# Optimization experiments

Measured on AMD Instinct MI355X. Metric: run time of the kernel, lower is better.

The kernel has to match this reference:

```python
import jax, jax.numpy as jnp
import numpy as np

N, T, D, H = 32, 1024, 1152, 16
DH = D // H            # 72
MLP = int(D * 4.0)     # 4608
EPS = 1e-6


def setup_inputs() -> dict:
    key = jax.random.key(0)
    ks = jax.random.split(key, 14)
    s = 0.02
    return {
        "x": jax.random.normal(ks[0], (N, T, D), jnp.float32),
        "c": jax.random.normal(ks[1], (N, D), jnp.float32),
        "qkv_w": jax.random.normal(ks[2], (D, 3 * D), jnp.float32) * s,
        "qkv_b": jax.random.normal(ks[3], (3 * D,), jnp.float32) * s,
        "proj_w": jax.random.normal(ks[4], (D, D), jnp.float32) * s,
        "proj_b": jax.random.normal(ks[5], (D,), jnp.float32) * s,
        "fc1_w": jax.random.normal(ks[6], (D, MLP), jnp.float32) * s,
        "fc1_b": jax.random.normal(ks[7], (MLP,), jnp.float32) * s,
        "fc2_w": jax.random.normal(ks[8], (MLP, D), jnp.float32) * s,
        "fc2_b": jax.random.normal(ks[9], (D,), jnp.float32) * s,
        "ada_w": jax.random.normal(ks[10], (D, 6 * D), jnp.float32) * s,
        "ada_b": jax.random.normal(ks[11], (6 * D,), jnp.float32) * s,
    }


def _layernorm(x):
    m = jnp.mean(x, axis=-1, keepdims=True)
    v = jnp.var(x, axis=-1, keepdims=True)
    return (x - m) * jax.lax.rsqrt(v + EPS)


def _modulate(x, shift, scale):
    # shift, scale: (N, D) broadcast over T
    return x * (1.0 + scale[:, None, :]) + shift[:, None, :]


def _attention(x, qkv_w, qkv_b, proj_w, proj_b):
    n, t, d = x.shape
    scale = DH ** (-0.5)
    qkv = x @ qkv_w + qkv_b                       # (N,T,3D)
    qkv = qkv.reshape(n, t, 3, H, DH)
    q, k, v = qkv[:, :, 0], qkv[:, :, 1], qkv[:, :, 2]  # each (N,T,H,DH)
    # Faithful to source: matmul over the LAST two dims -> per-token
    # head-vs-head attention of shape (N,T,H,H), softmax over heads.
    attn = jnp.einsum("nthd,ntkd->nthk", q * scale, k)
    attn = jax.nn.softmax(attn, axis=-1)
    out = jnp.einsum("nthk,ntkd->nthd", attn, v)  # (N,T,H,DH)
    out = out.transpose(0, 2, 1, 3).reshape(n, t, d)  # faithful scramble
    return out @ proj_w + proj_b


def _mlp(x, fc1_w, fc1_b, fc2_w, fc2_b):
    h = jax.nn.gelu(x @ fc1_w + fc1_b, approximate=False)  # exact GELU (torch default)
    return h @ fc2_w + fc2_b


def reference(x, c, qkv_w, qkv_b, proj_w, proj_b, fc1_w, fc1_b, fc2_w, fc2_b,
              ada_w, ada_b):
    ada = jax.nn.silu(c) @ ada_w + ada_b          # (N, 6D)
    (shift_msa, scale_msa, gate_msa,
     shift_mlp, scale_mlp, gate_mlp) = jnp.split(ada, 6, axis=1)
    x = x + gate_msa[:, None, :] * _attention(
        _modulate(_layernorm(x), shift_msa, scale_msa),
        qkv_w, qkv_b, proj_w, proj_b)
    x = x + gate_mlp[:, None, :] * _mlp(
        _modulate(_layernorm(x), shift_mlp, scale_mlp),
        fc1_w, fc1_b, fc2_w, fc2_b)
    return x
```

## Files before the change

kernel.cpp:

```cpp
#include <hip/hip_runtime.h>

#define DEV __device__ __forceinline__

typedef __attribute__((ext_vector_type(8))) short short8;
typedef __attribute__((ext_vector_type(8))) __bf16 bf16x8;
typedef __attribute__((ext_vector_type(4))) float f32x4;

#define TD      1024
#define DD      1152
#define DHH     72
#define MLPD    4608
#define QKVN    3456
#define ADAN    6912
#define MROWS   32768

DEV unsigned short f32_to_bf16(float f) {
  unsigned int u = __float_as_uint(f);
  u += 0x7fffu + ((u >> 16) & 1u);
  return (unsigned short)(u >> 16);
}

DEV void gl16(const void* g, void* l) {
  __builtin_amdgcn_global_load_lds((__attribute__((address_space(1))) void*)g,
                                   (__attribute__((address_space(3))) void*)l,
                                   16, 0, 0);
}

DEV bf16x8 zero_bf16x8() {
  short8 z = {0, 0, 0, 0, 0, 0, 0, 0};
  return __builtin_bit_cast(bf16x8, z);
}

DEV float gelu_exact(float v) {
  return 0.5f * v * (1.0f + erff(v * 0.70710678118654752f));
}

#define WAITV(n) asm volatile("s_waitcnt vmcnt(" #n ")" ::: "memory")

__global__ __launch_bounds__(256) void wtrans_kernel(const float* __restrict__ W,
                                                     unsigned short* __restrict__ Wt,
                                                     int K, int N) {
  __shared__ unsigned short tile[32][33];
  const int nb = blockIdx.x * 32, kb = blockIdx.y * 32;
  const int tx = threadIdx.x, ty = threadIdx.y;
  #pragma unroll
  for (int i = ty; i < 32; i += 8)
    tile[i][tx] = f32_to_bf16(W[(size_t)(kb + i) * N + nb + tx]);
  __syncthreads();
  #pragma unroll
  for (int i = ty; i < 32; i += 8)
    Wt[(size_t)(nb + i) * K + kb + tx] = tile[tx][i];
}

__global__ __launch_bounds__(256) void ada_kernel(const float* __restrict__ c,
                                                  const float* __restrict__ ada_w,
                                                  const float* __restrict__ ada_b,
                                                  float* __restrict__ ada_out) {
  __shared__ float sc[DD];
  const int n = blockIdx.y;
  const int col = blockIdx.x * 256 + threadIdx.x;
  for (int i = threadIdx.x; i < DD; i += 256) {
    float v = c[(size_t)n * DD + i];
    sc[i] = v / (1.0f + __expf(-v));
  }
  __syncthreads();
  float acc = ada_b[col];
  #pragma unroll 8
  for (int k = 0; k < DD; ++k)
    acc += sc[k] * ada_w[(size_t)k * ADAN + col];
  ada_out[(size_t)n * ADAN + col] = acc;
}

__global__ __launch_bounds__(256) void ln_mod_kernel(const float* __restrict__ X,
                                                     const float* __restrict__ ada,
                                                     int soff,
                                                     unsigned short* __restrict__ out) {
  const int row = blockIdx.x;
  const int batch = row >> 10;
  const float* xr = X + (size_t)row * DD;
  const int t = threadIdx.x;

  float4 v0 = reinterpret_cast<const float4*>(xr)[t];
  float4 v1 = make_float4(0.f, 0.f, 0.f, 0.f);
  const bool has2 = (t < 32);
  if (has2) v1 = reinterpret_cast<const float4*>(xr)[256 + t];

  float s  = v0.x + v0.y + v0.z + v0.w + v1.x + v1.y + v1.z + v1.w;
  float sq = v0.x*v0.x + v0.y*v0.y + v0.z*v0.z + v0.w*v0.w
           + v1.x*v1.x + v1.y*v1.y + v1.z*v1.z + v1.w*v1.w;
  #pragma unroll
  for (int m = 1; m < 64; m <<= 1) {
    s  += __shfl_xor(s, m);
    sq += __shfl_xor(sq, m);
  }
  __shared__ float red[8];
  const int wv = t >> 6;
  if ((t & 63) == 0) { red[wv] = s; red[4 + wv] = sq; }
  __syncthreads();
  s  = red[0] + red[1] + red[2] + red[3];
  sq = red[4] + red[5] + red[6] + red[7];
  const float mean = s * (1.0f / 1152.0f);
  const float var  = sq * (1.0f / 1152.0f) - mean * mean;
  const float rstd = rsqrtf(var + 1e-6f);

  const float* shp = ada + (size_t)batch * ADAN + soff;
  const float* scp = shp + DD;
  unsigned short* orow = out + (size_t)row * DD;

  {
    const int col = t * 4;
    ushort4 o4;
    o4.x = f32_to_bf16((v0.x - mean) * rstd * (1.0f + scp[col + 0]) + shp[col + 0]);
    o4.y = f32_to_bf16((v0.y - mean) * rstd * (1.0f + scp[col + 1]) + shp[col + 1]);
    o4.z = f32_to_bf16((v0.z - mean) * rstd * (1.0f + scp[col + 2]) + shp[col + 2]);
    o4.w = f32_to_bf16((v0.w - mean) * rstd * (1.0f + scp[col + 3]) + shp[col + 3]);
    reinterpret_cast<ushort4*>(orow)[t] = o4;
  }
  if (has2) {
    const int col = 1024 + t * 4;
    ushort4 o4;
    o4.x = f32_to_bf16((v1.x - mean) * rstd * (1.0f + scp[col + 0]) + shp[col + 0]);
    o4.y = f32_to_bf16((v1.y - mean) * rstd * (1.0f + scp[col + 1]) + shp[col + 1]);
    o4.z = f32_to_bf16((v1.z - mean) * rstd * (1.0f + scp[col + 2]) + shp[col + 2]);
    o4.w = f32_to_bf16((v1.w - mean) * rstd * (1.0f + scp[col + 3]) + shp[col + 3]);
    reinterpret_cast<ushort4*>(orow)[256 + t] = o4;
  }
}

template <int EPI>
__global__ __launch_bounds__(512) void gemm3b(
    const unsigned short* __restrict__ A, const unsigned short* __restrict__ Bt,
    const float* __restrict__ bias, const float* __restrict__ ada, int ada_off,
    const float* __restrict__ resid, unsigned short* __restrict__ out_bf,
    float* __restrict__ out_f, int N, int K, int ntn) {
  __shared__ unsigned short lds[24576];
  const int tid = threadIdx.x;
  const int lane = tid & 63, w = tid >> 6;
  const int wm = w >> 1, wn = w & 1;
  const int l15 = lane & 15, lg = lane >> 4;

  const int nwg = 128 * ntn, cpx = nwg >> 3;
  const int wg = (blockIdx.x & 7) * cpx + (blockIdx.x >> 3);
  const int bm = wg / ntn, bn = wg - bm * ntn;

  const unsigned short* __restrict__ Ag = A + (size_t)bm * 256 * K;
  const unsigned short* __restrict__ Bg = Bt + (size_t)bn * 128 * K;

  const int srow = tid >> 2;
  const int gch = ((tid & 3) ^ ((tid >> 3) & 3)) * 8;

#define STG(SL, KT) do {                                                                 \
    gl16(Ag + (size_t)srow * K + (size_t)(KT) * 32 + gch, &lds[(SL) + tid * 8]);         \
    gl16(Ag + (size_t)(srow + 128) * K + (size_t)(KT) * 32 + gch,                        \
         &lds[(SL) + 4096 + tid * 8]);                                                   \
    gl16(Bg + (size_t)srow * K + (size_t)(KT) * 32 + gch,                                \
         &lds[(SL) + 8192 + tid * 8]);                                                   \
  } while (0)

  const int chA = (lg ^ ((l15 >> 1) & 3)) * 8;
  const int arow0 = wm * 64 + l15;
  const int brow0 = wn * 64 + l15;

  f32x4 acc[4][4];
  #pragma unroll
  for (int m = 0; m < 4; ++m)
    #pragma unroll
    for (int nn = 0; nn < 4; ++nn)
      acc[m][nn] = (f32x4){0.f, 0.f, 0.f, 0.f};

  const int NT = K >> 5;

  STG(0, 0);
  for (int t = 0; t < NT; ++t) {
    const int sl = (t & 1) * 12288, ns = sl ^ 12288;
    if (t + 1 < NT) {
      STG(ns, t + 1);
      WAITV(3);
    } else {
      WAITV(0);
    }
    __builtin_amdgcn_s_barrier();

    const unsigned short* lb = lds + sl;
    bf16x8 af[4], bfv[4];
    #pragma unroll
    for (int mf = 0; mf < 4; ++mf)
      af[mf] = *(const bf16x8*)&lb[(arow0 + mf * 16) * 32 + chA];
    #pragma unroll
    for (int nf = 0; nf < 4; ++nf)
      bfv[nf] = *(const bf16x8*)&lb[8192 + (brow0 + nf * 16) * 32 + chA];
    __builtin_amdgcn_s_setprio(1);
    #pragma unroll
    for (int mf = 0; mf < 4; ++mf)
      #pragma unroll
      for (int nf = 0; nf < 4; ++nf)
        acc[mf][nf] = __builtin_amdgcn_mfma_f32_16x16x32_bf16(af[mf], bfv[nf], acc[mf][nf], 0, 0, 0);
    __builtin_amdgcn_s_setprio(0);
    __builtin_amdgcn_s_barrier();
  }
#undef STG

  const int batch = bm >> 2;
  const size_t row0 = (size_t)bm * 256 + wm * 64;
  const int col0 = bn * 128 + wn * 64;
  #pragma unroll
  for (int nf = 0; nf < 4; ++nf) {
    const int colg = col0 + nf * 16 + l15;
    const float bv = bias[colg];
    float g2 = 0.0f;
    if constexpr (EPI == 1 || EPI == 3) g2 = ada[(size_t)batch * ADAN + ada_off + colg];
    #pragma unroll
    for (int mf = 0; mf < 4; ++mf) {
      #pragma unroll
      for (int r = 0; r < 4; ++r) {
        const size_t idx = (row0 + mf * 16 + lg * 4 + r) * (size_t)N + colg;
        const float v = acc[mf][nf][r] + bv;
        if constexpr (EPI == 0)      out_bf[idx] = f32_to_bf16(v);
        else if constexpr (EPI == 2) out_bf[idx] = f32_to_bf16(gelu_exact(v));
        else if constexpr (EPI == 1) out_f[idx] = resid[idx] + g2 * v;
        else                         out_f[idx] = out_f[idx] + g2 * v;
      }
    }
  }
}

__global__ __launch_bounds__(256) void attn_kernel(const unsigned short* __restrict__ qkv,
                                                   unsigned short* __restrict__ y) {
  const int tid = threadIdx.x, w = tid >> 6, lane = tid & 63;
  const int l15 = lane & 15, lg = lane >> 4;
  const int tok = blockIdx.x * 4 + w;
  const int n = tok >> 10, t = tok & 1023;

  __shared__ unsigned short Pl[4][16 * 32];
  __shared__ unsigned short Vl[4][16 * 80];

  for (int i = lane; i < 16 * 32; i += 64)
    if ((i & 31) >= 16) Pl[w][i] = 0;

  const size_t rowb = (size_t)tok * QKVN;
  const float scale = 0.11785113019775793f;

  bf16x8 aq[3];
  #pragma unroll
  for (int kk = 0; kk < 3; ++kk) {
    const int d0 = kk * 32 + lg * 8;
    aq[kk] = (d0 < DHH) ? *(const bf16x8*)&qkv[rowb + l15 * DHH + d0] : zero_bf16x8();
  }

  for (int c = lane; c < 144; c += 64) {
    const int r = c / 9, cc = (c % 9) * 8;
    *(short8*)&Vl[w][r * 80 + cc] = *(const short8*)&qkv[rowb + 2 * DD + r * DHH + cc];
  }

  f32x4 s = (f32x4){0.f, 0.f, 0.f, 0.f};
  #pragma unroll
  for (int kk = 0; kk < 3; ++kk) {
    const int d0 = kk * 32 + lg * 8;
    bf16x8 bk = (d0 < DHH) ? *(const bf16x8*)&qkv[rowb + DD + l15 * DHH + d0] : zero_bf16x8();
    s = __builtin_amdgcn_mfma_f32_16x16x32_bf16(aq[kk], bk, s, 0, 0, 0);
  }

  float p[4], mx[4], ssum[4];
  #pragma unroll
  for (int r = 0; r < 4; ++r) { p[r] = s[r] * scale; mx[r] = p[r]; }
  #pragma unroll
  for (int mk = 1; mk <= 8; mk <<= 1)
    #pragma unroll
    for (int r = 0; r < 4; ++r) mx[r] = fmaxf(mx[r], __shfl_xor(mx[r], mk));
  #pragma unroll
  for (int r = 0; r < 4; ++r) { p[r] = __expf(p[r] - mx[r]); ssum[r] = p[r]; }
  #pragma unroll
  for (int mk = 1; mk <= 8; mk <<= 1)
    #pragma unroll
    for (int r = 0; r < 4; ++r) ssum[r] += __shfl_xor(ssum[r], mk);

  #pragma unroll
  for (int r = 0; r < 4; ++r)
    Pl[w][(lg * 4 + r) * 32 + l15] = f32_to_bf16(p[r] / ssum[r]);

  bf16x8 pa = *(const bf16x8*)&Pl[w][l15 * 32 + lg * 8];
  const int kb = (lg & 1) * 8;
  f32x4 o[5];
  #pragma unroll
  for (int df = 0; df < 5; ++df) {
    short8 bvv;
    #pragma unroll
    for (int j = 0; j < 8; ++j)
      bvv[j] = (short)Vl[w][(kb + j) * 80 + df * 16 + l15];
    o[df] = __builtin_amdgcn_mfma_f32_16x16x32_bf16(
        pa, __builtin_bit_cast(bf16x8, bvv), (f32x4){0.f, 0.f, 0.f, 0.f}, 0, 0, 0);
  }

  unsigned short* yb = y + (size_t)n * (TD * DD);
  #pragma unroll
  for (int df = 0; df < 5; ++df) {
    const int d = df * 16 + l15;
    if (d < DHH) {
      #pragma unroll
      for (int r = 0; r < 4; ++r) {
        const int h = lg * 4 + r;
        yb[h * 73728 + t * DHH + d] = f32_to_bf16(o[df][r]);
      }
    }
  }
}

extern "C" void kernel_launch(void* const* d_in, const int* in_sizes, int n_in,
                              void* d_out, int out_size, void* d_ws, size_t ws_size,
                              hipStream_t stream) {
  (void)in_sizes; (void)n_in; (void)out_size; (void)ws_size;
  const float* x      = (const float*)d_in[0];
  const float* c      = (const float*)d_in[1];
  const float* qkv_w  = (const float*)d_in[2];
  const float* qkv_b  = (const float*)d_in[3];
  const float* proj_w = (const float*)d_in[4];
  const float* proj_b = (const float*)d_in[5];
  const float* fc1_w  = (const float*)d_in[6];
  const float* fc1_b  = (const float*)d_in[7];
  const float* fc2_w  = (const float*)d_in[8];
  const float* fc2_b  = (const float*)d_in[9];
  const float* ada_w  = (const float*)d_in[10];
  const float* ada_b  = (const float*)d_in[11];
  float* out = (float*)d_out;

  char* ws = (char*)d_ws;
  unsigned short* hbuf    = (unsigned short*)ws;
  unsigned short* qkvbuf  = hbuf;
  unsigned short* attnbuf = hbuf + (size_t)MROWS * QKVN;
  size_t off = 301989888ull;
  unsigned short* xm    = (unsigned short*)(ws + off); off += 75497472ull;
  unsigned short* wtq   = (unsigned short*)(ws + off); off += (size_t)QKVN * DD * 2;
  unsigned short* wtp   = (unsigned short*)(ws + off); off += (size_t)DD * DD * 2;
  unsigned short* wtf1  = (unsigned short*)(ws + off); off += (size_t)MLPD * DD * 2;
  unsigned short* wtf2  = (unsigned short*)(ws + off); off += (size_t)DD * MLPD * 2;
  float*          adab  = (float*)(ws + off); off += 884736ull;

  const dim3 tb(32, 8);
  hipLaunchKernelGGL(wtrans_kernel, dim3(QKVN / 32, DD / 32), tb, 0, stream, qkv_w, wtq, DD, QKVN);
  hipLaunchKernelGGL(wtrans_kernel, dim3(DD / 32, DD / 32),   tb, 0, stream, proj_w, wtp, DD, DD);
  hipLaunchKernelGGL(wtrans_kernel, dim3(MLPD / 32, DD / 32), tb, 0, stream, fc1_w, wtf1, DD, MLPD);
  hipLaunchKernelGGL(wtrans_kernel, dim3(DD / 32, MLPD / 32), tb, 0, stream, fc2_w, wtf2, MLPD, DD);

  hipLaunchKernelGGL(ada_kernel, dim3(ADAN / 256, 32), dim3(256), 0, stream, c, ada_w, ada_b, adab);

  hipLaunchKernelGGL(ln_mod_kernel, dim3(MROWS), dim3(256), 0, stream, x, adab, 0, xm);

  hipLaunchKernelGGL((gemm3b<0>), dim3(128 * 27), dim3(512), 0, stream,
                     xm, wtq, qkv_b, nullptr, 0, nullptr, qkvbuf, nullptr, QKVN, DD, 27);

  hipLaunchKernelGGL(attn_kernel, dim3(MROWS / 4), dim3(256), 0, stream, qkvbuf, attnbuf);

  hipLaunchKernelGGL((gemm3b<1>), dim3(128 * 9), dim3(512), 0, stream,
                     attnbuf, wtp, proj_b, adab, 2304, x, nullptr, out, DD, DD, 9);

  hipLaunchKernelGGL(ln_mod_kernel, dim3(MROWS), dim3(256), 0, stream, out, adab, 3456, xm);

  hipLaunchKernelGGL((gemm3b<2>), dim3(128 * 36), dim3(512), 0, stream,
                     xm, wtf1, fc1_b, nullptr, 0, nullptr, hbuf, nullptr, MLPD, DD, 36);

  hipLaunchKernelGGL((gemm3b<3>), dim3(128 * 9), dim3(512), 0, stream,
                     hbuf, wtf2, fc2_b, adab, 5760, nullptr, nullptr, out, DD, MLPD, 9);
}
```

Baseline: 1.755 ms.

## Use 256x256-tile 16-wave GEMM kernel for the MLP fc1/fc2 matmuls

Adds a new GEMM kernel with 1024-thread workgroups (16 waves) computing 256x256 output tiles with double-buffered LDS staging, and uses it for fc1 and fc2 instead of the previous 512-thread kernel. Larger tiles raise arithmetic intensity and cut global/L2 traffic per FLOP. fc2's N=1152 is not a multiple of 256, so five column tiles are used, the transposed weight buffer is padded to 1280 rows, and out-of-range columns are skipped in the epilogue. The padded weight rows are never written, so those lanes compute on garbage that is discarded. The larger workgroups risk lower occupancy and wasted work on the partial fc2 tile.

```diff
diff --git a/kernel.cpp b/kernel.cpp
--- a/kernel.cpp
+++ b/kernel.cpp
@@ -124,6 +124,103 @@
     o4.z = f32_to_bf16((v1.z - mean) * rstd * (1.0f + scp[col + 2]) + shp[col + 2]);
     o4.w = f32_to_bf16((v1.w - mean) * rstd * (1.0f + scp[col + 3]) + shp[col + 3]);
     reinterpret_cast<ushort4*>(orow)[256 + t] = o4;
+  }
+}
+
+template <int EPI>
+__global__ __launch_bounds__(1024) void gemm16w(
+    const unsigned short* __restrict__ A, const unsigned short* __restrict__ Bt,
+    const float* __restrict__ bias, const float* __restrict__ ada, int ada_off,
+    const float* __restrict__ resid, unsigned short* __restrict__ out_bf,
+    float* __restrict__ out_f, int N, int K, int ntn) {
+  __shared__ unsigned short lds[32768];
+  const int tid = threadIdx.x;
+  const int lane = tid & 63, w = tid >> 6;
+  const int wm = w >> 2, wn = w & 3;
+  const int l15 = lane & 15, lg = lane >> 4;
+
+  const int nwg = 128 * ntn, cpx = nwg >> 3;
+  const int wg = (blockIdx.x & 7) * cpx + (blockIdx.x >> 3);
+  const int bm = wg / ntn, bn = wg - bm * ntn;
+
+  const unsigned short* __restrict__ Ag = A + (size_t)bm * 256 * K;
+  const unsigned short* __restrict__ Bg = Bt + (size_t)bn * 256 * K;
+
+  const int srow = tid >> 2;
+  const int gch = ((tid & 3) ^ ((tid >> 3) & 3)) * 8;
+
+#define STG(SL, KT) do {                                                                 \
+    gl16(Ag + (size_t)srow * K + (size_t)(KT) * 32 + gch, &lds[(SL) + tid * 8]);         \
+    gl16(Bg + (size_t)srow * K + (size_t)(KT) * 32 + gch,                                \
+         &lds[(SL) + 8192 + tid * 8]);                                                   \
+  } while (0)
+
+  const int chA = (lg ^ ((l15 >> 1) & 3)) * 8;
+  const int arow0 = wm * 64 + l15;
+  const int brow0 = wn * 64 + l15;
+
+  f32x4 acc[4][4];
+  #pragma unroll
+  for (int m = 0; m < 4; ++m)
+    #pragma unroll
+    for (int nn = 0; nn < 4; ++nn)
+      acc[m][nn] = (f32x4){0.f, 0.f, 0.f, 0.f};
+
+  const int NT = K >> 5;
+
+  STG(0, 0);
+  for (int t = 0; t < NT; ++t) {
+    const int sl = (t & 1) << 14, ns = sl ^ 16384;
+    if (t + 1 < NT) {
+      STG(ns, t + 1);
+      WAITV(2);
+    } else {
+      WAITV(0);
+    }
+    __builtin_amdgcn_s_barrier();
+
+    const unsigned short* lb = lds + sl;
+    bf16x8 af[4], bfv[4];
+    #pragma unroll
+    for (int mf = 0; mf < 4; ++mf)
+      af[mf] = *(const bf16x8*)&lb[(arow0 + mf * 16) * 32 + chA];
+    #pragma unroll
+    for (int nf = 0; nf < 4; ++nf)
+      bfv[nf] = *(const bf16x8*)&lb[8192 + (brow0 + nf * 16) * 32 + chA];
+    __builtin_amdgcn_s_setprio(1);
+    #pragma unroll
+    for (int mf = 0; mf < 4; ++mf)
+      #pragma unroll
+      for (int nf = 0; nf < 4; ++nf)
+        acc[mf][nf] = __builtin_amdgcn_mfma_f32_16x16x32_bf16(af[mf], bfv[nf], acc[mf][nf], 0, 0, 0);
+    __builtin_amdgcn_s_setprio(0);
+    __builtin_amdgcn_s_barrier();
+  }
+#undef STG
+
+  const int batch = bm >> 2;
+  const size_t row0 = (size_t)bm * 256 + wm * 64;
+  const int col0 = bn * 256 + wn * 64;
+  #pragma unroll
+  for (int nf = 0; nf < 4; ++nf) {
+    const int colb = col0 + nf * 16;
+    if (colb >= N) continue;
+    const int colg = colb + l15;
+    const float bv = bias[colg];
+    float g2 = 0.0f;
+    if constexpr (EPI == 1 || EPI == 3) g2 = ada[(size_t)batch * ADAN + ada_off + colg];
+    #pragma unroll
+    for (int mf = 0; mf < 4; ++mf) {
+      #pragma unroll
+      for (int r = 0; r < 4; ++r) {
+        const size_t idx = (row0 + mf * 16 + lg * 4 + r) * (size_t)N + colg;
+        const float v = acc[mf][nf][r] + bv;
+        if constexpr (EPI == 0)      out_bf[idx] = f32_to_bf16(v);
+        else if constexpr (EPI == 2) out_bf[idx] = f32_to_bf16(gelu_exact(v));
+        else if constexpr (EPI == 1) out_f[idx] = resid[idx] + g2 * v;
+        else                         out_f[idx] = out_f[idx] + g2 * v;
+      }
+    }
   }
 }
 
@@ -332,7 +429,7 @@
   unsigned short* wtq   = (unsigned short*)(ws + off); off += (size_t)QKVN * DD * 2;
   unsigned short* wtp   = (unsigned short*)(ws + off); off += (size_t)DD * DD * 2;
   unsigned short* wtf1  = (unsigned short*)(ws + off); off += (size_t)MLPD * DD * 2;
-  unsigned short* wtf2  = (unsigned short*)(ws + off); off += (size_t)DD * MLPD * 2;
+  unsigned short* wtf2  = (unsigned short*)(ws + off); off += (size_t)1280 * MLPD * 2;
   float*          adab  = (float*)(ws + off); off += 884736ull;
 
   const dim3 tb(32, 8);
@@ -355,9 +452,9 @@
 
   hipLaunchKernelGGL(ln_mod_kernel, dim3(MROWS), dim3(256), 0, stream, out, adab, 3456, xm);
 
-  hipLaunchKernelGGL((gemm3b<2>), dim3(128 * 36), dim3(512), 0, stream,
-                     xm, wtf1, fc1_b, nullptr, 0, nullptr, hbuf, nullptr, MLPD, DD, 36);
-
-  hipLaunchKernelGGL((gemm3b<3>), dim3(128 * 9), dim3(512), 0, stream,
-                     hbuf, wtf2, fc2_b, adab, 5760, nullptr, nullptr, out, DD, MLPD, 9);
-}
+  hipLaunchKernelGGL((gemm16w<2>), dim3(128 * 18), dim3(1024), 0, stream,
+                     xm, wtf1, fc1_b, nullptr, 0, nullptr, hbuf, nullptr, MLPD, DD, 18);
+
+  hipLaunchKernelGGL((gemm16w<3>), dim3(128 * 5), dim3(1024), 0, stream,
+                     hbuf, wtf2, fc2_b, adab, 5760, nullptr, nullptr, out, DD, MLPD, 5);
+}
```

After: 1.822 ms. +3.8%, slower.
